# Optimization experiments

Hardware: AMD Instinct MI355X
Metric: run time of the kernel (lower is better)

## Reference

```python
import jax, jax.numpy as jnp
import numpy as np

# mamba-2.8b layer dims
B_, L = 2, 2048
D_MODEL = 2560
D_IN = 2 * D_MODEL          # 5120, d_inner
N = 16                      # d_state
DT_RANK = D_MODEL // 16     # 160


def setup_inputs() -> dict:
    key = jax.random.key(0)
    ks = jax.random.split(key, 6)
    x = jax.random.normal(ks[0], (B_, L, D_IN), dtype=jnp.float32)
    # A_log initialized so A = -exp(A_log) in [-16, -1], as in Mamba's S4D-real init
    A_log = jnp.log(jax.random.uniform(ks[1], (D_IN, N), minval=1.0, maxval=16.0, dtype=jnp.float32))
    D = jax.random.normal(ks[2], (D_IN,), dtype=jnp.float32) * 0.1 + 1.0
    x_proj_w = jax.random.normal(ks[3], (DT_RANK + 2 * N, D_IN), dtype=jnp.float32) * (D_IN ** -0.5)
    dt_proj_w = jax.random.normal(ks[4], (D_IN, DT_RANK), dtype=jnp.float32) * (DT_RANK ** -0.5)
    dt_proj_b = jax.random.normal(ks[5], (D_IN,), dtype=jnp.float32) * 0.1
    return {"x": x, "A_log": A_log, "D": D, "x_proj_w": x_proj_w,
            "dt_proj_w": dt_proj_w, "dt_proj_b": dt_proj_b}


def _ssm(x, A_log, D, x_proj_w, dt_proj_w, dt_proj_b):
    # x: (b, l, d_inner)
    A = -jnp.exp(A_log)                                        # (d, n)
    x_dbl = jnp.einsum('bld,ed->ble', x, x_proj_w)             # (b, l, dt_rank+2n)
    dt_raw = x_dbl[..., :DT_RANK]                              # (b, l, dt_rank)
    Bm = x_dbl[..., DT_RANK:DT_RANK + N]                       # (b, l, n)
    Cm = x_dbl[..., DT_RANK + N:]                              # (b, l, n)
    delta = jax.nn.softplus(jnp.einsum('blr,dr->bld', dt_raw, dt_proj_w) + dt_proj_b)  # (b, l, d)

    def step(h, inp):
        xt, dt, Bt, Ct = inp                                   # (b,d) (b,d) (b,n) (b,n)
        dA = jnp.exp(dt[..., None] * A)                        # (b, d, n)
        h = dA * h + (dt * xt)[..., None] * Bt[:, None, :]     # (b, d, n)
        y = jnp.einsum('bdn,bn->bd', h, Ct)                    # (b, d)
        return h, y

    xs = (jnp.swapaxes(x, 0, 1), jnp.swapaxes(delta, 0, 1),
          jnp.swapaxes(Bm, 0, 1), jnp.swapaxes(Cm, 0, 1))
    h0 = jnp.zeros((x.shape[0], D_IN, N), dtype=x.dtype)
    _, ys = jax.lax.scan(step, h0, xs)                         # ys: (l, b, d)
    return jnp.swapaxes(ys, 0, 1) + x * D                      # (b, l, d)


def reference(x, A_log, D, x_proj_w, dt_proj_w, dt_proj_b):
    return _ssm(x, A_log, D, x_proj_w, dt_proj_w, dt_proj_b)
```

## Files before the change

kernel.cpp:

```cpp
#include <hip/hip_runtime.h>
#include <hip/hip_bf16.h>

#define DIN   5120
#define LSEQ  2048
#define BATCH 2
#define MROWS 4096
#define EOUT  192
#define RDT   160
#define NST   16
#define NC    32
#define LC    64
#define LOG2E 1.44269504088896f
#define LN2   0.69314718055995f

typedef __attribute__((ext_vector_type(8))) short bf16x8;
typedef __attribute__((ext_vector_type(4))) float f32x4;

__device__ __forceinline__ void stdelta(float* p, size_t i, float v) { p[i] = v; }
__device__ __forceinline__ void stdelta(__hip_bfloat16* p, size_t i, float v) { p[i] = __float2bfloat16(v); }
__device__ __forceinline__ float lddelta(const float* p, size_t i) { return p[i]; }
__device__ __forceinline__ float lddelta(const __hip_bfloat16* p, size_t i) { return __bfloat162float(p[i]); }

__device__ __forceinline__ float softplus_fast(float v) {
    float t = __builtin_amdgcn_exp2f(-fabsf(v) * LOG2E);
    return fmaxf(v, 0.f) + __builtin_amdgcn_logf(1.f + t) * LN2;
}
__device__ __forceinline__ unsigned short bf16rne(float f) {
    unsigned int u = __float_as_uint(f);
    unsigned int r = (u + 0x7FFFu + ((u >> 16) & 1u)) >> 16;
    return (unsigned short)r;
}
__device__ __forceinline__ void cvt8(float4 a, float4 b, bf16x8& h, bf16x8& l) {
    float v[8] = {a.x, a.y, a.z, a.w, b.x, b.y, b.z, b.w};
    #pragma unroll
    for (int e = 0; e < 8; e++) {
        unsigned int u = __float_as_uint(v[e]);
        unsigned int hb = u & 0xFFFF0000u;
        h[e] = (short)(hb >> 16);
        l[e] = (short)bf16rne(v[e] - __uint_as_float(hb));
    }
}

__global__ void k0_cvtw(const float* __restrict__ w, ushort* __restrict__ bw) {
    int i = blockIdx.x * 256 + threadIdx.x;
    float4 v = reinterpret_cast<const float4*>(w)[i];
    ushort4 o = make_ushort4(bf16rne(v.x), bf16rne(v.y), bf16rne(v.z), bf16rne(v.w));
    reinterpret_cast<ushort4*>(bw)[i] = o;
}

template <int KPS>
__global__ __launch_bounds__(256) void k1_mfma(const float* __restrict__ x,
                                               const ushort* __restrict__ bWp,
                                               float* __restrict__ part) {
    const int tid = threadIdx.x;
    const int m_base = blockIdx.x * 128;
    const int k_base = blockIdx.y * KPS;
    const int lane = tid & 63, w = tid >> 6;
    const int lr = lane & 15, lg = lane >> 4;
    const int wm = m_base + w * 32;

    f32x4 acc[2][12];
    #pragma unroll
    for (int i = 0; i < 2; i++)
        #pragma unroll
        for (int j = 0; j < 12; j++) acc[i][j] = (f32x4)(0.f);

    const float* xr0 = x + (size_t)(wm + lr) * DIN + k_base;
    const float* xr1 = x + (size_t)(wm + 16 + lr) * DIN + k_base;

    #pragma unroll 2
    for (int kk = 0; kk < KPS / 32; kk++) {
        const int ko = kk * 32 + lg * 8;
        float4 v0 = *reinterpret_cast<const float4*>(xr0 + ko);
        float4 v1 = *reinterpret_cast<const float4*>(xr0 + ko + 4);
        float4 v2 = *reinterpret_cast<const float4*>(xr1 + ko);
        float4 v3 = *reinterpret_cast<const float4*>(xr1 + ko + 4);
        bf16x8 ah0, al0, ah1, al1;
        cvt8(v0, v1, ah0, al0);
        cvt8(v2, v3, ah1, al1);
        #pragma unroll
        for (int j = 0; j < 12; j++) {
            bf16x8 bb = *reinterpret_cast<const bf16x8*>(bWp + (size_t)(j * 16 + lr) * DIN + k_base + ko);
            acc[0][j] = __builtin_amdgcn_mfma_f32_16x16x32_bf16(ah0, bb, acc[0][j], 0, 0, 0);
            acc[1][j] = __builtin_amdgcn_mfma_f32_16x16x32_bf16(ah1, bb, acc[1][j], 0, 0, 0);
            acc[0][j] = __builtin_amdgcn_mfma_f32_16x16x32_bf16(al0, bb, acc[0][j], 0, 0, 0);
            acc[1][j] = __builtin_amdgcn_mfma_f32_16x16x32_bf16(al1, bb, acc[1][j], 0, 0, 0);
        }
    }
    float* p = part + (size_t)blockIdx.y * MROWS * EOUT;
    #pragma unroll
    for (int j = 0; j < 12; j++) {
        const int e = j * 16 + lr;
        #pragma unroll
        for (int i = 0; i < 2; i++) {
            const int m0 = wm + i * 16 + lg * 4;
            #pragma unroll
            for (int r = 0; r < 4; r++)
                p[(size_t)(m0 + r) * EOUT + e] = acc[i][j][r];
        }
    }
}

template <int KS>
__global__ void k1_reduce(const float* __restrict__ part, float* __restrict__ xdbl,
                          ushort* __restrict__ aHi, ushort* __restrict__ aLo) {
    int i = blockIdx.x * 256 + threadIdx.x;
    const float4* p = reinterpret_cast<const float4*>(part);
    float4 s = p[i];
    #pragma unroll
    for (int k = 1; k < KS; k++) {
        float4 v = p[(size_t)k * (MROWS * EOUT / 4) + i];
        s.x += v.x; s.y += v.y; s.z += v.z; s.w += v.w;
    }
    reinterpret_cast<float4*>(xdbl)[i] = s;
    int row = i / 48, e4 = i % 48;
    if (e4 < 40) {
        unsigned int hx = __float_as_uint(s.x) & 0xFFFF0000u;
        unsigned int hy = __float_as_uint(s.y) & 0xFFFF0000u;
        unsigned int hz = __float_as_uint(s.z) & 0xFFFF0000u;
        unsigned int hw = __float_as_uint(s.w) & 0xFFFF0000u;
        ushort4 hv = make_ushort4((unsigned short)(hx >> 16), (unsigned short)(hy >> 16),
                                  (unsigned short)(hz >> 16), (unsigned short)(hw >> 16));
        ushort4 lv = make_ushort4(bf16rne(s.x - __uint_as_float(hx)),
                                  bf16rne(s.y - __uint_as_float(hy)),
                                  bf16rne(s.z - __uint_as_float(hz)),
                                  bf16rne(s.w - __uint_as_float(hw)));
        *reinterpret_cast<ushort4*>(&aHi[(size_t)row * RDT + e4 * 4]) = hv;
        *reinterpret_cast<ushort4*>(&aLo[(size_t)row * RDT + e4 * 4]) = lv;
    }
}

template <typename DT>
__global__ __launch_bounds__(256, 3) void k2_mfma(const ushort* __restrict__ aHi,
                                                  const ushort* __restrict__ aLo,
                                                  const ushort* __restrict__ bW,
                                                  const float* __restrict__ bias,
                                                  DT* __restrict__ delta) {
    const int tid = threadIdx.x;
    const int m_base = blockIdx.x * 64, d_base = blockIdx.y * 256;
    const int lane = tid & 63, w = tid >> 6;
    const int wr = w >> 1, wc = w & 1;
    const int lr = lane & 15, lg = lane >> 4;

    f32x4 acc[2][8];
    #pragma unroll
    for (int i = 0; i < 2; i++)
        #pragma unroll
        for (int j = 0; j < 8; j++) acc[i][j] = (f32x4)(0.f);

    const size_t arow = (size_t)(m_base + wr * 32 + lr) * RDT;
    const size_t brow = (size_t)(d_base + wc * 128 + lr) * RDT;

    #pragma unroll
    for (int kk = 0; kk < 5; kk++) {
        const int ko = kk * 32 + lg * 8;
        bf16x8 ah0 = *reinterpret_cast<const bf16x8*>(aHi + arow + ko);
        bf16x8 ah1 = *reinterpret_cast<const bf16x8*>(aHi + arow + 16 * RDT + ko);
        bf16x8 al0 = *reinterpret_cast<const bf16x8*>(aLo + arow + ko);
        bf16x8 al1 = *reinterpret_cast<const bf16x8*>(aLo + arow + 16 * RDT + ko);
        #pragma unroll
        for (int j = 0; j < 8; j++) {
            bf16x8 bb = *reinterpret_cast<const bf16x8*>(bW + brow + (size_t)j * 16 * RDT + ko);
            acc[0][j] = __builtin_amdgcn_mfma_f32_16x16x32_bf16(ah0, bb, acc[0][j], 0, 0, 0);
            acc[1][j] = __builtin_amdgcn_mfma_f32_16x16x32_bf16(ah1, bb, acc[1][j], 0, 0, 0);
            acc[0][j] = __builtin_amdgcn_mfma_f32_16x16x32_bf16(al0, bb, acc[0][j], 0, 0, 0);
            acc[1][j] = __builtin_amdgcn_mfma_f32_16x16x32_bf16(al1, bb, acc[1][j], 0, 0, 0);
        }
    }

    #pragma unroll
    for (int j = 0; j < 8; j++) {
        const int gd = d_base + wc * 128 + j * 16 + lr;
        const float bv = bias[gd];
        #pragma unroll
        for (int i = 0; i < 2; i++) {
            const int gm0 = m_base + wr * 32 + i * 16 + lg * 4;
            #pragma unroll
            for (int r = 0; r < 4; r++) {
                float v = acc[i][j][r] + bv;
                stdelta(delta, (size_t)(gm0 + r) * DIN + gd, softplus_fast(v));
            }
        }
    }
}

template <typename DT>
__global__ __launch_bounds__(256) void k3a_local(const float* __restrict__ x,
                                                 const DT* __restrict__ delta,
                                                 const float* __restrict__ xdbl,
                                                 const float* __restrict__ A_log,
                                                 float* __restrict__ Sbuf,
                                                 float* __restrict__ hend0) {
    __shared__ float4 Bs[LC][4];
    const int tid = threadIdx.x;
    const int d = blockIdx.x * 256 + tid;
    const int c = blockIdx.y, b = blockIdx.z;

    {
        int t = tid >> 2, q = tid & 3;
        const float* row = xdbl + ((size_t)b * LSEQ + (size_t)c * LC + t) * EOUT + RDT;
        Bs[t][q] = *reinterpret_cast<const float4*>(row + q * 4);
    }

    float4 aq[4];
    #pragma unroll
    for (int q = 0; q < 4; q++) aq[q] = *reinterpret_cast<const float4*>(&A_log[d * NST + q * 4]);
    const float* av = reinterpret_cast<const float*>(aq);
    float A2[NST];
    #pragma unroll
    for (int n = 0; n < NST; n++) A2[n] = -expf(av[n]) * LOG2E;

    float h[NST];
    #pragma unroll
    for (int n = 0; n < NST; n++) h[n] = 0.f;
    float S = 0.f;

    const size_t gbase = (size_t)b * LSEQ * DIN + (size_t)c * LC * DIN + d;
    float dv = lddelta(delta, gbase);
    float xv = x[gbase];
    __syncthreads();

    for (int tt = 0; tt < LC; tt++) {
        const int ttn = (tt + 1 < LC) ? tt + 1 : tt;
        float dv_n = lddelta(delta, gbase + (size_t)ttn * DIN);
        float xv_n = x[gbase + (size_t)ttn * DIN];
        float4 bv[4];
        bv[0] = Bs[tt][0]; bv[1] = Bs[tt][1]; bv[2] = Bs[tt][2]; bv[3] = Bs[tt][3];
        const float* Bv = reinterpret_cast<const float*>(bv);
        S += dv;
        const float dvx = dv * xv;
        #pragma unroll
        for (int n = 0; n < NST; n++)
            h[n] = fmaf(__builtin_amdgcn_exp2f(dv * A2[n]), h[n], dvx * Bv[n]);
        dv = dv_n; xv = xv_n;
    }
    Sbuf[((size_t)b * NC + c) * DIN + d] = S;
    float* hp = hend0 + (((size_t)b * NC + c) * DIN + d) * NST;
    #pragma unroll
    for (int q = 0; q < 4; q++)
        reinterpret_cast<float4*>(hp)[q] = make_float4(h[q*4], h[q*4+1], h[q*4+2], h[q*4+3]);
}

__global__ __launch_bounds__(256) void k3b_combine(const float* __restrict__ Sbuf,
                                                   const float* __restrict__ hend0,
                                                   const float* __restrict__ A_log,
                                                   float* __restrict__ hinit) {
    const int i = blockIdx.x * 256 + threadIdx.x;
    const int b = i / (DIN * 4);
    const int r = i % (DIN * 4);
    const int d = r >> 2, q = r & 3;
    float4 av = *reinterpret_cast<const float4*>(&A_log[d * NST + q * 4]);
    float A2x = -expf(av.x) * LOG2E, A2y = -expf(av.y) * LOG2E;
    float A2z = -expf(av.z) * LOG2E, A2w = -expf(av.w) * LOG2E;
    float4 hi = make_float4(0.f, 0.f, 0.f, 0.f);
    for (int c = 0; c < NC; c++) {
        const size_t idx4 = (((size_t)b * NC + c) * DIN + d) * 4 + q;
        reinterpret_cast<float4*>(hinit)[idx4] = hi;
        float S = Sbuf[((size_t)b * NC + c) * DIN + d];
        float4 he = reinterpret_cast<const float4*>(hend0)[idx4];
        hi.x = fmaf(__builtin_amdgcn_exp2f(S * A2x), hi.x, he.x);
        hi.y = fmaf(__builtin_amdgcn_exp2f(S * A2y), hi.y, he.y);
        hi.z = fmaf(__builtin_amdgcn_exp2f(S * A2z), hi.z, he.z);
        hi.w = fmaf(__builtin_amdgcn_exp2f(S * A2w), hi.w, he.w);
    }
}

template <typename DT>
__global__ __launch_bounds__(256) void k3c_scan(const float* __restrict__ x,
                                                const DT* __restrict__ delta,
                                                const float* __restrict__ xdbl,
                                                const float* __restrict__ A_log,
                                                const float* __restrict__ Dw,
                                                const float* __restrict__ hinit,
                                                float* __restrict__ out) {
    __shared__ float4 BCs[LC][8];
    const int tid = threadIdx.x;
    const int d = blockIdx.x * 256 + tid;
    const int c = blockIdx.y, b = blockIdx.z;

    {
        #pragma unroll
        for (int it = 0; it < 2; it++) {
            int pi = tid + it * 256;
            int t = pi >> 3, q = pi & 7;
            const float* row = xdbl + ((size_t)b * LSEQ + (size_t)c * LC + t) * EOUT + RDT;
            BCs[t][q] = *reinterpret_cast<const float4*>(row + q * 4);
        }
    }

    float4 aq[4];
    #pragma unroll
    for (int q = 0; q < 4; q++) aq[q] = *reinterpret_cast<const float4*>(&A_log[d * NST + q * 4]);
    const float* av = reinterpret_cast<const float*>(aq);
    float A2[NST];
    #pragma unroll
    for (int n = 0; n < NST; n++) A2[n] = -expf(av[n]) * LOG2E;

    float h[NST];
    {
        const float* hp = hinit + (((size_t)b * NC + c) * DIN + d) * NST;
        float4 hq[4];
        #pragma unroll
        for (int q = 0; q < 4; q++) hq[q] = reinterpret_cast<const float4*>(hp)[q];
        const float* hv = reinterpret_cast<const float*>(hq);
        #pragma unroll
        for (int n = 0; n < NST; n++) h[n] = hv[n];
    }
    const float Dv = Dw[d];

    const size_t gbase = (size_t)b * LSEQ * DIN + (size_t)c * LC * DIN + d;
    float dv = lddelta(delta, gbase);
    float xv = x[gbase];
    __syncthreads();

    for (int tt = 0; tt < LC; tt++) {
        const int ttn = (tt + 1 < LC) ? tt + 1 : tt;
        float dv_n = lddelta(delta, gbase + (size_t)ttn * DIN);
        float xv_n = x[gbase + (size_t)ttn * DIN];
        float4 bv[4], cv[4];
        bv[0] = BCs[tt][0]; bv[1] = BCs[tt][1]; bv[2] = BCs[tt][2]; bv[3] = BCs[tt][3];
        cv[0] = BCs[tt][4]; cv[1] = BCs[tt][5]; cv[2] = BCs[tt][6]; cv[3] = BCs[tt][7];
        const float* Bv = reinterpret_cast<const float*>(bv);
        const float* Cv = reinterpret_cast<const float*>(cv);
        const float dvx = dv * xv;
        float y0 = 0.f, y1 = 0.f, y2 = 0.f, y3 = 0.f;
        #pragma unroll
        for (int n = 0; n < NST; n += 4) {
            h[n+0] = fmaf(__builtin_amdgcn_exp2f(dv * A2[n+0]), h[n+0], dvx * Bv[n+0]);
            y0 = fmaf(h[n+0], Cv[n+0], y0);
            h[n+1] = fmaf(__builtin_amdgcn_exp2f(dv * A2[n+1]), h[n+1], dvx * Bv[n+1]);
            y1 = fmaf(h[n+1], Cv[n+1], y1);
            h[n+2] = fmaf(__builtin_amdgcn_exp2f(dv * A2[n+2]), h[n+2], dvx * Bv[n+2]);
            y2 = fmaf(h[n+2], Cv[n+2], y2);
            h[n+3] = fmaf(__builtin_amdgcn_exp2f(dv * A2[n+3]), h[n+3], dvx * Bv[n+3]);
            y3 = fmaf(h[n+3], Cv[n+3], y3);
        }
        out[gbase + (size_t)tt * DIN] = ((y0 + y1) + (y2 + y3)) + xv * Dv;
        dv = dv_n; xv = xv_n;
    }
}

extern "C" void kernel_launch(void* const* d_in, const int* in_sizes, int n_in,
                              void* d_out, int out_size, void* d_ws, size_t ws_size,
                              hipStream_t stream) {
    const float* x     = (const float*)d_in[0];
    const float* A_log = (const float*)d_in[1];
    const float* Dw    = (const float*)d_in[2];
    const float* xpw   = (const float*)d_in[3];
    const float* dtw   = (const float*)d_in[4];
    const float* dtb   = (const float*)d_in[5];
    float* out = (float*)d_out;

    char* ws = (char*)d_ws;
    size_t off = 0;
    float* xdbl  = (float*)(ws + off); off += (size_t)MROWS * EOUT * 4;
    float* hend0 = (float*)(ws + off); off += (size_t)BATCH * NC * DIN * NST * 4;
    float* hinit = (float*)(ws + off); off += (size_t)BATCH * NC * DIN * NST * 4;
    float* Sbuf  = (float*)(ws + off); off += (size_t)BATCH * NC * DIN * 4;
    ushort* aHi  = (ushort*)(ws + off); off += (size_t)MROWS * RDT * 2;
    ushort* aLo  = (ushort*)(ws + off); off += (size_t)MROWS * RDT * 2;
    ushort* bW   = (ushort*)(ws + off); off += (size_t)DIN * RDT * 2;
    ushort* bWp  = (ushort*)(ws + off); off += (size_t)EOUT * DIN * 2;
    const size_t delta_off = off;
    const bool f32ok = ws_size >= delta_off + (size_t)MROWS * DIN * 4;

    k0_cvtw<<<dim3(EOUT * DIN / 4 / 256), 256, 0, stream>>>(xpw, bWp);
    k0_cvtw<<<dim3(DIN * RDT / 4 / 256), 256, 0, stream>>>(dtw, bW);

    if (f32ok) {
        float* part = (float*)(ws + delta_off);
        float* delta = (float*)(ws + delta_off);
        k1_mfma<DIN / 16><<<dim3(MROWS / 128, 16), 256, 0, stream>>>(x, bWp, part);
        k1_reduce<16><<<dim3(MROWS * EOUT / 4 / 256), 256, 0, stream>>>(part, xdbl, aHi, aLo);
        k2_mfma<float><<<dim3(MROWS / 64, DIN / 256), 256, 0, stream>>>(aHi, aLo, bW, dtb, delta);
        k3a_local<float><<<dim3(DIN / 256, NC, BATCH), 256, 0, stream>>>(x, delta, xdbl, A_log, Sbuf, hend0);
        k3b_combine<<<dim3(BATCH * DIN * 4 / 256), 256, 0, stream>>>(Sbuf, hend0, A_log, hinit);
        k3c_scan<float><<<dim3(DIN / 256, NC, BATCH), 256, 0, stream>>>(x, delta, xdbl, A_log, Dw, hinit, out);
    } else {
        float* part = hend0;
        __hip_bfloat16* delta = (__hip_bfloat16*)(ws + delta_off);
        k1_mfma<DIN / 8><<<dim3(MROWS / 128, 8), 256, 0, stream>>>(x, bWp, part);
        k1_reduce<8><<<dim3(MROWS * EOUT / 4 / 256), 256, 0, stream>>>(part, xdbl, aHi, aLo);
        k2_mfma<__hip_bfloat16><<<dim3(MROWS / 64, DIN / 256), 256, 0, stream>>>(aHi, aLo, bW, dtb, delta);
        k3a_local<__hip_bfloat16><<<dim3(DIN / 256, NC, BATCH), 256, 0, stream>>>(x, delta, xdbl, A_log, Sbuf, hend0);
        k3b_combine<<<dim3(BATCH * DIN * 4 / 256), 256, 0, stream>>>(Sbuf, hend0, A_log, hinit);
        k3c_scan<__hip_bfloat16><<<dim3(DIN / 256, NC, BATCH), 256, 0, stream>>>(x, delta, xdbl, A_log, Dw, hinit, out);
    }
}
```

Before: 246.8 us.

## Split SSM state across thread pairs and drop shared-memory B/C staging

The chunked scan kernels now assign two threads per channel, each owning 8 of the 16 state elements. This doubles the thread count and halves the per-thread serial work and register load. B and C are no longer staged in shared memory with a block barrier; each thread prefetches its slice straight from global memory one step ahead. The y partial sums are combined with a lane shuffle. In exchange, the delta and x loads are duplicated across each pair, B/C global loads happen every step, and only half the lanes write outputs.

```diff
diff --git a/kernel.cpp b/kernel.cpp
--- a/kernel.cpp
+++ b/kernel.cpp
@@ -191,54 +191,44 @@
                                                  const float* __restrict__ A_log,
                                                  float* __restrict__ Sbuf,
                                                  float* __restrict__ hend0) {
-    __shared__ float4 Bs[LC][4];
     const int tid = threadIdx.x;
-    const int d = blockIdx.x * 256 + tid;
+    const int half = tid & 1;
+    const int d = blockIdx.x * 128 + (tid >> 1);
     const int c = blockIdx.y, b = blockIdx.z;
 
-    {
-        int t = tid >> 2, q = tid & 3;
-        const float* row = xdbl + ((size_t)b * LSEQ + (size_t)c * LC + t) * EOUT + RDT;
-        Bs[t][q] = *reinterpret_cast<const float4*>(row + q * 4);
-    }
-
-    float4 aq[4];
-    #pragma unroll
-    for (int q = 0; q < 4; q++) aq[q] = *reinterpret_cast<const float4*>(&A_log[d * NST + q * 4]);
-    const float* av = reinterpret_cast<const float*>(aq);
-    float A2[NST];
-    #pragma unroll
-    for (int n = 0; n < NST; n++) A2[n] = -expf(av[n]) * LOG2E;
-
-    float h[NST];
-    #pragma unroll
-    for (int n = 0; n < NST; n++) h[n] = 0.f;
+    float4 a0 = *reinterpret_cast<const float4*>(&A_log[d * NST + half * 8]);
+    float4 a1 = *reinterpret_cast<const float4*>(&A_log[d * NST + half * 8 + 4]);
+    float A2[8] = {a0.x, a0.y, a0.z, a0.w, a1.x, a1.y, a1.z, a1.w};
+    #pragma unroll
+    for (int n = 0; n < 8; n++) A2[n] = -expf(A2[n]) * LOG2E;
+
+    float h[8] = {0.f, 0.f, 0.f, 0.f, 0.f, 0.f, 0.f, 0.f};
     float S = 0.f;
-
     const size_t gbase = (size_t)b * LSEQ * DIN + (size_t)c * LC * DIN + d;
+    const float* Bb = xdbl + ((size_t)b * LSEQ + (size_t)c * LC) * EOUT + RDT + half * 8;
+
     float dv = lddelta(delta, gbase);
     float xv = x[gbase];
-    __syncthreads();
-
+    float4 b0 = *reinterpret_cast<const float4*>(Bb);
+    float4 b1 = *reinterpret_cast<const float4*>(Bb + 4);
     for (int tt = 0; tt < LC; tt++) {
         const int ttn = (tt + 1 < LC) ? tt + 1 : tt;
-        float dv_n = lddelta(delta, gbase + (size_t)ttn * DIN);
-        float xv_n = x[gbase + (size_t)ttn * DIN];
-        float4 bv[4];
-        bv[0] = Bs[tt][0]; bv[1] = Bs[tt][1]; bv[2] = Bs[tt][2]; bv[3] = Bs[tt][3];
-        const float* Bv = reinterpret_cast<const float*>(bv);
+        float dvn = lddelta(delta, gbase + (size_t)ttn * DIN);
+        float xvn = x[gbase + (size_t)ttn * DIN];
+        float4 b0n = *reinterpret_cast<const float4*>(Bb + (size_t)ttn * EOUT);
+        float4 b1n = *reinterpret_cast<const float4*>(Bb + (size_t)ttn * EOUT + 4);
+        const float Bv[8] = {b0.x, b0.y, b0.z, b0.w, b1.x, b1.y, b1.z, b1.w};
         S += dv;
         const float dvx = dv * xv;
         #pragma unroll
-        for (int n = 0; n < NST; n++)
+        for (int n = 0; n < 8; n++)
             h[n] = fmaf(__builtin_amdgcn_exp2f(dv * A2[n]), h[n], dvx * Bv[n]);
-        dv = dv_n; xv = xv_n;
-    }
-    Sbuf[((size_t)b * NC + c) * DIN + d] = S;
-    float* hp = hend0 + (((size_t)b * NC + c) * DIN + d) * NST;
-    #pragma unroll
-    for (int q = 0; q < 4; q++)
-        reinterpret_cast<float4*>(hp)[q] = make_float4(h[q*4], h[q*4+1], h[q*4+2], h[q*4+3]);
+        dv = dvn; xv = xvn; b0 = b0n; b1 = b1n;
+    }
+    if (half == 0) Sbuf[((size_t)b * NC + c) * DIN + d] = S;
+    float* hp = hend0 + (((size_t)b * NC + c) * DIN + d) * NST + half * 8;
+    *reinterpret_cast<float4*>(hp)     = make_float4(h[0], h[1], h[2], h[3]);
+    *reinterpret_cast<float4*>(hp + 4) = make_float4(h[4], h[5], h[6], h[7]);
 }
 
 __global__ __launch_bounds__(256) void k3b_combine(const float* __restrict__ Sbuf,
@@ -273,70 +263,59 @@
                                                 const float* __restrict__ Dw,
                                                 const float* __restrict__ hinit,
                                                 float* __restrict__ out) {
-    __shared__ float4 BCs[LC][8];
     const int tid = threadIdx.x;
-    const int d = blockIdx.x * 256 + tid;
+    const int half = tid & 1;
+    const int d = blockIdx.x * 128 + (tid >> 1);
     const int c = blockIdx.y, b = blockIdx.z;
 
+    float4 a0 = *reinterpret_cast<const float4*>(&A_log[d * NST + half * 8]);
+    float4 a1 = *reinterpret_cast<const float4*>(&A_log[d * NST + half * 8 + 4]);
+    float A2[8] = {a0.x, a0.y, a0.z, a0.w, a1.x, a1.y, a1.z, a1.w};
+    #pragma unroll
+    for (int n = 0; n < 8; n++) A2[n] = -expf(A2[n]) * LOG2E;
+
+    float h[8];
     {
-        #pragma unroll
-        for (int it = 0; it < 2; it++) {
-            int pi = tid + it * 256;
-            int t = pi >> 3, q = pi & 7;
-            const float* row = xdbl + ((size_t)b * LSEQ + (size_t)c * LC + t) * EOUT + RDT;
-            BCs[t][q] = *reinterpret_cast<const float4*>(row + q * 4);
-        }
-    }
-
-    float4 aq[4];
-    #pragma unroll
-    for (int q = 0; q < 4; q++) aq[q] = *reinterpret_cast<const float4*>(&A_log[d * NST + q * 4]);
-    const float* av = reinterpret_cast<const float*>(aq);
-    float A2[NST];
-    #pragma unroll
-    for (int n = 0; n < NST; n++) A2[n] = -expf(av[n]) * LOG2E;
-
-    float h[NST];
-    {
-        const float* hp = hinit + (((size_t)b * NC + c) * DIN + d) * NST;
-        float4 hq[4];
-        #pragma unroll
-        for (int q = 0; q < 4; q++) hq[q] = reinterpret_cast<const float4*>(hp)[q];
-        const float* hv = reinterpret_cast<const float*>(hq);
-        #pragma unroll
-        for (int n = 0; n < NST; n++) h[n] = hv[n];
+        const float* hp = hinit + (((size_t)b * NC + c) * DIN + d) * NST + half * 8;
+        float4 h0 = *reinterpret_cast<const float4*>(hp);
+        float4 h1 = *reinterpret_cast<const float4*>(hp + 4);
+        h[0] = h0.x; h[1] = h0.y; h[2] = h0.z; h[3] = h0.w;
+        h[4] = h1.x; h[5] = h1.y; h[6] = h1.z; h[7] = h1.w;
     }
     const float Dv = Dw[d];
 
     const size_t gbase = (size_t)b * LSEQ * DIN + (size_t)c * LC * DIN + d;
+    const float* Bb = xdbl + ((size_t)b * LSEQ + (size_t)c * LC) * EOUT + RDT + half * 8;
+
     float dv = lddelta(delta, gbase);
     float xv = x[gbase];
-    __syncthreads();
-
+    float4 b0 = *reinterpret_cast<const float4*>(Bb);
+    float4 b1 = *reinterpret_cast<const float4*>(Bb + 4);
+    float4 c0 = *reinterpret_cast<const float4*>(Bb + NST);
+    float4 c1 = *reinterpret_cast<const float4*>(Bb + NST + 4);
     for (int tt = 0; tt < LC; tt++) {
         const int ttn = (tt + 1 < LC) ? tt + 1 : tt;
-        float dv_n = lddelta(delta, gbase + (size_t)ttn * DIN);
-        float xv_n = x[gbase + (size_t)ttn * DIN];
-        float4 bv[4], cv[4];
-        bv[0] = BCs[tt][0]; bv[1] = BCs[tt][1]; bv[2] = BCs[tt][2]; bv[3] = BCs[tt][3];
-        cv[0] = BCs[tt][4]; cv[1] = BCs[tt][5]; cv[2] = BCs[tt][6]; cv[3] = BCs[tt][7];
-        const float* Bv = reinterpret_cast<const float*>(bv);
-        const float* Cv = reinterpret_cast<const float*>(cv);
+        float dvn = lddelta(delta, gbase + (size_t)ttn * DIN);
+        float xvn = x[gbase + (size_t)ttn * DIN];
+        float4 b0n = *reinterpret_cast<const float4*>(Bb + (size_t)ttn * EOUT);
+        float4 b1n = *reinterpret_cast<const float4*>(Bb + (size_t)ttn * EOUT + 4);
+        float4 c0n = *reinterpret_cast<const float4*>(Bb + (size_t)ttn * EOUT + NST);
+        float4 c1n = *reinterpret_cast<const float4*>(Bb + (size_t)ttn * EOUT + NST + 4);
+        const float Bv[8] = {b0.x, b0.y, b0.z, b0.w, b1.x, b1.y, b1.z, b1.w};
+        const float Cv[8] = {c0.x, c0.y, c0.z, c0.w, c1.x, c1.y, c1.z, c1.w};
         const float dvx = dv * xv;
-        float y0 = 0.f, y1 = 0.f, y2 = 0.f, y3 = 0.f;
-        #pragma unroll
-        for (int n = 0; n < NST; n += 4) {
-            h[n+0] = fmaf(__builtin_amdgcn_exp2f(dv * A2[n+0]), h[n+0], dvx * Bv[n+0]);
-            y0 = fmaf(h[n+0], Cv[n+0], y0);
+        float y0 = 0.f, y1 = 0.f;
+        #pragma unroll
+        for (int n = 0; n < 8; n += 2) {
+            h[n]   = fmaf(__builtin_amdgcn_exp2f(dv * A2[n]),   h[n],   dvx * Bv[n]);
+            y0 = fmaf(h[n],   Cv[n],   y0);
             h[n+1] = fmaf(__builtin_amdgcn_exp2f(dv * A2[n+1]), h[n+1], dvx * Bv[n+1]);
             y1 = fmaf(h[n+1], Cv[n+1], y1);
-            h[n+2] = fmaf(__builtin_amdgcn_exp2f(dv * A2[n+2]), h[n+2], dvx * Bv[n+2]);
-            y2 = fmaf(h[n+2], Cv[n+2], y2);
-            h[n+3] = fmaf(__builtin_amdgcn_exp2f(dv * A2[n+3]), h[n+3], dvx * Bv[n+3]);
-            y3 = fmaf(h[n+3], Cv[n+3], y3);
-        }
-        out[gbase + (size_t)tt * DIN] = ((y0 + y1) + (y2 + y3)) + xv * Dv;
-        dv = dv_n; xv = xv_n;
+        }
+        float y = y0 + y1;
+        y += __shfl_xor(y, 1);
+        if (half == 0) out[gbase + (size_t)tt * DIN] = y + xv * Dv;
+        dv = dvn; xv = xvn; b0 = b0n; b1 = b1n; c0 = c0n; c1 = c1n;
     }
 }
 
@@ -373,17 +352,17 @@
         k1_mfma<DIN / 16><<<dim3(MROWS / 128, 16), 256, 0, stream>>>(x, bWp, part);
         k1_reduce<16><<<dim3(MROWS * EOUT / 4 / 256), 256, 0, stream>>>(part, xdbl, aHi, aLo);
         k2_mfma<float><<<dim3(MROWS / 64, DIN / 256), 256, 0, stream>>>(aHi, aLo, bW, dtb, delta);
-        k3a_local<float><<<dim3(DIN / 256, NC, BATCH), 256, 0, stream>>>(x, delta, xdbl, A_log, Sbuf, hend0);
+        k3a_local<float><<<dim3(DIN / 128, NC, BATCH), 256, 0, stream>>>(x, delta, xdbl, A_log, Sbuf, hend0);
         k3b_combine<<<dim3(BATCH * DIN * 4 / 256), 256, 0, stream>>>(Sbuf, hend0, A_log, hinit);
-        k3c_scan<float><<<dim3(DIN / 256, NC, BATCH), 256, 0, stream>>>(x, delta, xdbl, A_log, Dw, hinit, out);
+        k3c_scan<float><<<dim3(DIN / 128, NC, BATCH), 256, 0, stream>>>(x, delta, xdbl, A_log, Dw, hinit, out);
     } else {
         float* part = hend0;
         __hip_bfloat16* delta = (__hip_bfloat16*)(ws + delta_off);
         k1_mfma<DIN / 8><<<dim3(MROWS / 128, 8), 256, 0, stream>>>(x, bWp, part);
         k1_reduce<8><<<dim3(MROWS * EOUT / 4 / 256), 256, 0, stream>>>(part, xdbl, aHi, aLo);
         k2_mfma<__hip_bfloat16><<<dim3(MROWS / 64, DIN / 256), 256, 0, stream>>>(aHi, aLo, bW, dtb, delta);
-        k3a_local<__hip_bfloat16><<<dim3(DIN / 256, NC, BATCH), 256, 0, stream>>>(x, delta, xdbl, A_log, Sbuf, hend0);
+        k3a_local<__hip_bfloat16><<<dim3(DIN / 128, NC, BATCH), 256, 0, stream>>>(x, delta, xdbl, A_log, Sbuf, hend0);
         k3b_combine<<<dim3(BATCH * DIN * 4 / 256), 256, 0, stream>>>(Sbuf, hend0, A_log, hinit);
-        k3c_scan<__hip_bfloat16><<<dim3(DIN / 256, NC, BATCH), 256, 0, stream>>>(x, delta, xdbl, A_log, Dw, hinit, out);
-    }
-}
+        k3c_scan<__hip_bfloat16><<<dim3(DIN / 128, NC, BATCH), 256, 0, stream>>>(x, delta, xdbl, A_log, Dw, hinit, out);
+    }
+}
```

Measured after the change: 280.6 us. 13.7% more time.
